# Performance work log

Measured on AMD Instinct MI355X. Metric: run time of the kernel, lower is better.

Reference implementation:

```python
import jax, jax.numpy as jnp
import numpy as np

N = 50000      # nodes
IN = 256       # in_feat
H = 4          # num_heads
DH = 64        # out_feat // num_heads
R = 6          # number of relations
E = 300000     # edges per relation
NEG_SLOPE = 0.2  # DGL GATConv leaky_relu slope


def setup_inputs() -> dict:
    key = jax.random.key(0)
    ks = jax.random.split(key, 7)
    x = jax.random.normal(ks[0], (N, IN), dtype=jnp.float32)
    W = jax.random.normal(ks[1], (R, IN, H * DH), dtype=jnp.float32) * (1.0 / np.sqrt(IN))
    attn_l = jax.random.normal(ks[2], (R, H, DH), dtype=jnp.float32) * 0.1
    attn_r = jax.random.normal(ks[3], (R, H, DH), dtype=jnp.float32) * 0.1
    bias = jax.random.normal(ks[4], (R, H * DH), dtype=jnp.float32) * 0.01
    src = jax.random.randint(ks[5], (R, E), 0, N, dtype=jnp.int32).astype(jnp.int64)
    dst = jax.random.randint(ks[6], (R, E), 0, N, dtype=jnp.int32).astype(jnp.int64)
    return {"x": x, "W": W, "attn_l": attn_l, "attn_r": attn_r, "bias": bias,
            "src": src, "dst": dst}


def reference(x, W, attn_l, attn_r, bias, src, dst):
    n = x.shape[0]
    r_total, h, dh = attn_l.shape
    out = jnp.zeros((n, h, dh), dtype=x.dtype)
    # small fixed loop over structurally-distinct relations (HeteroGraphConv)
    for r in range(r_total):
        feat = (x @ W[r]).reshape(n, h, dh)            # [N,H,Dh] shared src/dst proj
        el = jnp.sum(feat * attn_l[r], axis=-1)        # [N,H]
        er = jnp.sum(feat * attn_r[r], axis=-1)        # [N,H]
        s, d = src[r], dst[r]
        e = jax.nn.leaky_relu(el[s] + er[d], NEG_SLOPE)  # [E,H]
        # segmented softmax over incoming edges of each dst node
        m = jax.ops.segment_max(e, d, num_segments=n)    # [N,H]
        m = jnp.where(jnp.isfinite(m), m, 0.0)
        a = jnp.exp(e - m[d])                            # [E,H]
        z = jax.ops.segment_sum(a, d, num_segments=n)    # [N,H]
        alpha = a / jnp.maximum(z[d], 1e-9)              # [E,H]
        msg = alpha[:, :, None] * feat[s]                # [E,H,Dh]
        agg = jax.ops.segment_sum(msg, d, num_segments=n)  # [N,H,Dh]
        # GATConv: bias + activation(relu) per relation, HeteroGraphConv sums
        out = out + jax.nn.relu(agg + bias[r].reshape(h, dh))
    hcat = out.reshape(n, h * dh)                        # merge='cat' view
    return jax.nn.relu(hcat)                             # layer-level activation
```

## Files before the change

### kernel.cpp

```cpp
#include <hip/hip_runtime.h>

#define NN 50000
#define MP 50048
#define NH 4
#define NR 6
#define NE 300000
#define HD 256
#define SLOTS 32
#define CHUNKS 64
#define CHSZ ((NE + CHUNKS - 1) / CHUNKS)

typedef __attribute__((ext_vector_type(4))) float f32x4;
typedef __attribute__((ext_vector_type(8))) short bf16x8;

__device__ __forceinline__ short f2bf(float f) {
  unsigned u = __float_as_uint(f);
  unsigned r = (u + 0x7FFFu + ((u >> 16) & 1u)) >> 16;
  return (short)r;
}
__device__ __forceinline__ float bf2f_lo(unsigned d) {
  return __uint_as_float(d << 16);
}
__device__ __forceinline__ float bf2f_hi(unsigned d) {
  return __uint_as_float(d & 0xffff0000u);
}

#define GLOAD_LDS16(g, l)                                                     \
  __builtin_amdgcn_global_load_lds(                                           \
      (const __attribute__((address_space(1))) void*)(g),                     \
      (__attribute__((address_space(3))) void*)(l), 16, 0, 0)

__global__ __launch_bounds__(256) void cast_x_kernel(
    const float* __restrict__ x, short* __restrict__ xb, int n4) {
  const int i = blockIdx.x * 256 + threadIdx.x;
  if (i >= n4) return;
  const float4 v = ((const float4*)x)[i];
  short4 o;
  o.x = f2bf(v.x); o.y = f2bf(v.y); o.z = f2bf(v.z); o.w = f2bf(v.w);
  ((short4*)xb)[i] = o;
}

__global__ __launch_bounds__(256) void cast_wt_kernel(
    const float* __restrict__ W, short* __restrict__ wt) {
  const int o = blockIdx.x * 256 + threadIdx.x;
  if (o >= NR * 256 * 256) return;
  const int r = o >> 16;
  const int nrow = (o >> 8) & 255;
  const int k = o & 255;
  wt[o] = f2bf(W[r * 65536 + k * 256 + nrow]);
}

__global__ __launch_bounds__(256) void gemm_kernel(
    const short* __restrict__ xb,
    const short* __restrict__ wt_all,
    const float* __restrict__ attn_l,
    const float* __restrict__ attn_r,
    short* __restrict__ featb_all,
    float* __restrict__ el_all, float* __restrict__ er_all) {
  __shared__ short As[128 * 32];
  __shared__ short Bs[128 * 32];
  const int t = threadIdx.x;
  const int lane = t & 63;
  const int w = t >> 6;
  const int wm = w & 1, wn = w >> 1;
  const int row0 = blockIdx.x * 128;
  const int n0 = blockIdx.y * 128;
  const int r = blockIdx.z;
  const short* wt = wt_all + (size_t)r * 65536;
  short* featb = featb_all + (size_t)r * MP * 256;

  f32x4 acc[4][4];
#pragma unroll
  for (int mi = 0; mi < 4; ++mi)
#pragma unroll
    for (int ni = 0; ni < 4; ++ni) {
      f32x4 z = {0.f, 0.f, 0.f, 0.f};
      acc[mi][ni] = z;
    }

  const int c0 = t, c1 = 256 + t;
  int ar0 = row0 + (c0 >> 2); if (ar0 >= NN) ar0 = NN - 1;
  int ar1 = row0 + (c1 >> 2); if (ar1 >= NN) ar1 = NN - 1;
  const short* ag0 = xb + (size_t)ar0 * 256 + (c0 & 3) * 8;
  const short* ag1 = xb + (size_t)ar1 * 256 + (c1 & 3) * 8;
  const short* bg0 = wt + (size_t)(n0 + (c0 >> 2)) * 256 + (c0 & 3) * 8;
  const short* bg1 = wt + (size_t)(n0 + (c1 >> 2)) * 256 + (c1 & 3) * 8;
  short* la0 = As + c0 * 8;
  short* la1 = As + c1 * 8;
  short* lb0 = Bs + c0 * 8;
  short* lb1 = Bs + c1 * 8;

  const int ra = lane & 15;
  const int qa = (lane >> 4) * 8;

  for (int k0 = 0; k0 < 256; k0 += 32) {
    GLOAD_LDS16(ag0 + k0, la0);
    GLOAD_LDS16(ag1 + k0, la1);
    GLOAD_LDS16(bg0 + k0, lb0);
    GLOAD_LDS16(bg1 + k0, lb1);
    __syncthreads();
    bf16x8 af[4], bfr[4];
#pragma unroll
    for (int mi = 0; mi < 4; ++mi)
      af[mi] = *(const bf16x8*)&As[(wm * 64 + mi * 16 + ra) * 32 + qa];
#pragma unroll
    for (int ni = 0; ni < 4; ++ni)
      bfr[ni] = *(const bf16x8*)&Bs[(wn * 64 + ni * 16 + ra) * 32 + qa];
#pragma unroll
    for (int mi = 0; mi < 4; ++mi)
#pragma unroll
      for (int ni = 0; ni < 4; ++ni)
        acc[mi][ni] = __builtin_amdgcn_mfma_f32_16x16x32_bf16(
            af[mi], bfr[ni], acc[mi][ni], 0, 0, 0);
    __syncthreads();
  }

  const int h = (n0 >> 6) + wn;
  float alv[4], arv[4];
#pragma unroll
  for (int ni = 0; ni < 4; ++ni) {
    alv[ni] = attn_l[r * HD + h * 64 + ni * 16 + ra];
    arv[ni] = attn_r[r * HD + h * 64 + ni * 16 + ra];
  }
#pragma unroll
  for (int mi = 0; mi < 4; ++mi) {
#pragma unroll
    for (int j = 0; j < 4; ++j) {
      const int row = row0 + wm * 64 + mi * 16 + (lane >> 4) * 4 + j;
      float elp = 0.f, erp = 0.f;
#pragma unroll
      for (int ni = 0; ni < 4; ++ni) {
        const float v = acc[mi][ni][j];
        featb[(size_t)row * 256 + n0 + wn * 64 + ni * 16 + ra] = f2bf(v);
        elp = fmaf(v, alv[ni], elp);
        erp = fmaf(v, arv[ni], erp);
      }
#pragma unroll
      for (int m = 1; m < 16; m <<= 1) {
        elp += __shfl_xor(elp, m, 64);
        erp += __shfl_xor(erp, m, 64);
      }
      if (ra == 0 && row < NN) {
        el_all[((size_t)r * NN + row) * NH + h] = elp;
        er_all[((size_t)r * NN + row) * NH + h] = erp;
      }
    }
  }
}

__global__ __launch_bounds__(256) void pack_kernel(
    const int* __restrict__ src, const int* __restrict__ dst,
    unsigned* __restrict__ pe) {
  const int i = blockIdx.x * 256 + threadIdx.x;
  if (i < NR * NE)
    pe[i] = ((unsigned)dst[i] << 16) | (unsigned)src[i];
}

__global__ __launch_bounds__(256) void build_kernel(
    const unsigned* __restrict__ pe, int* __restrict__ deg,
    unsigned short* __restrict__ slots) {
  const int grp = blockIdx.x & 7;
  const int chunk = blockIdx.x >> 3;
  const int lo = chunk * CHSZ;
  const int hi = (lo + CHSZ < NE) ? lo + CHSZ : NE;
  const unsigned dlo = grp * (NN / 8);
  for (int r = 0; r < NR; ++r) {
    for (int i = lo + threadIdx.x; i < hi; i += 256) {
      const unsigned p = pe[(size_t)r * NE + i];
      const unsigned d = p >> 16;
      if (d - dlo < (unsigned)(NN / 8)) {
        const int g = r * NN + (int)d;
        const int sl = atomicAdd(&deg[g], 1);
        if (sl < SLOTS)
          slots[(size_t)g * SLOTS + sl] = (unsigned short)(p & 0xffffu);
      }
    }
  }
}

__global__ __launch_bounds__(256) void agg_kernel(
    const short* __restrict__ featb_all, const float* __restrict__ el_all,
    const float* __restrict__ er_all, const int* __restrict__ deg,
    const unsigned short* __restrict__ slots, const float* __restrict__ bias,
    float* __restrict__ out) {
  const int wid = (blockIdx.x * 256 + threadIdx.x) >> 6;
  const int lane = threadIdx.x & 63;
  if (wid >= NN) return;
  const int h = lane >> 4;
  const int c0 = lane * 4;

  float oacc[4] = {0.f, 0.f, 0.f, 0.f};
  const int wid_u = __builtin_amdgcn_readfirstlane(wid);

  for (int r = 0; r < NR; ++r) {
    const int g = r * NN + wid_u;
    int dg = __builtin_amdgcn_readfirstlane(deg[g]);
    dg = dg > SLOTS ? SLOTS : dg;
    const uint4* sp = (const uint4*)(slots + (size_t)g * SLOTS);
    const uint4 q0 = sp[0], q1 = sp[1], q2 = sp[2], q3 = sp[3];
    unsigned sdv[16];
    sdv[0]  = __builtin_amdgcn_readfirstlane(q0.x);
    sdv[1]  = __builtin_amdgcn_readfirstlane(q0.y);
    sdv[2]  = __builtin_amdgcn_readfirstlane(q0.z);
    sdv[3]  = __builtin_amdgcn_readfirstlane(q0.w);
    sdv[4]  = __builtin_amdgcn_readfirstlane(q1.x);
    sdv[5]  = __builtin_amdgcn_readfirstlane(q1.y);
    sdv[6]  = __builtin_amdgcn_readfirstlane(q1.z);
    sdv[7]  = __builtin_amdgcn_readfirstlane(q1.w);
    sdv[8]  = __builtin_amdgcn_readfirstlane(q2.x);
    sdv[9]  = __builtin_amdgcn_readfirstlane(q2.y);
    sdv[10] = __builtin_amdgcn_readfirstlane(q2.z);
    sdv[11] = __builtin_amdgcn_readfirstlane(q2.w);
    sdv[12] = __builtin_amdgcn_readfirstlane(q3.x);
    sdv[13] = __builtin_amdgcn_readfirstlane(q3.y);
    sdv[14] = __builtin_amdgcn_readfirstlane(q3.z);
    sdv[15] = __builtin_amdgcn_readfirstlane(q3.w);

    const float er_nh = er_all[(size_t)g * NH + h];
    const float* elr = el_all + (size_t)r * NN * NH;
    const short* fb = featb_all + (size_t)r * MP * 256;

    float z = 0.f;
    float acc[4] = {0.f, 0.f, 0.f, 0.f};

#pragma unroll
    for (int j0 = 0; j0 < SLOTS; j0 += 4) {
      if (j0 >= dg) break;
      float pv[4];
      uint2 rw[4];
#pragma unroll
      for (int k = 0; k < 4; ++k) {
        const int e = j0 + k;
        int s = (int)((e & 1) ? (sdv[e >> 1] >> 16) : (sdv[e >> 1] & 0xffffu));
        const bool v = e < dg;
        s = v ? s : 0;
        rw[k] = *(const uint2*)(fb + (size_t)s * 256 + c0);
        float ev = elr[s * NH + h] + er_nh;
        ev = fmaxf(ev, 0.2f * ev);
        pv[k] = v ? __expf(ev) : 0.f;
      }
#pragma unroll
      for (int k = 0; k < 4; ++k) {
        z += pv[k];
        acc[0] = fmaf(pv[k], bf2f_lo(rw[k].x), acc[0]);
        acc[1] = fmaf(pv[k], bf2f_hi(rw[k].x), acc[1]);
        acc[2] = fmaf(pv[k], bf2f_lo(rw[k].y), acc[2]);
        acc[3] = fmaf(pv[k], bf2f_hi(rw[k].y), acc[3]);
      }
    }

    const float inv = 1.f / fmaxf(z, 1e-9f);
    const float4 bv = *(const float4*)(bias + r * HD + c0);
    oacc[0] += fmaxf(fmaf(acc[0], inv, bv.x), 0.f);
    oacc[1] += fmaxf(fmaf(acc[1], inv, bv.y), 0.f);
    oacc[2] += fmaxf(fmaf(acc[2], inv, bv.z), 0.f);
    oacc[3] += fmaxf(fmaf(acc[3], inv, bv.w), 0.f);
  }

  float4 o4 = {oacc[0], oacc[1], oacc[2], oacc[3]};
  *(float4*)(out + (size_t)wid * 256 + c0) = o4;
}

extern "C" void kernel_launch(void* const* d_in, const int* in_sizes, int n_in,
                              void* d_out, int out_size, void* d_ws,
                              size_t ws_size, hipStream_t stream) {
  const float* x      = (const float*)d_in[0];
  const float* W      = (const float*)d_in[1];
  const float* attn_l = (const float*)d_in[2];
  const float* attn_r = (const float*)d_in[3];
  const float* bias   = (const float*)d_in[4];
  const int*   src    = (const int*)d_in[5];
  const int*   dst    = (const int*)d_in[6];
  float* out = (float*)d_out;

  char* p = (char*)d_ws;
  auto alloc = [&](size_t bytes) {
    char* r = p;
    p += (bytes + 255) & ~(size_t)255;
    return r;
  };
  short* xb    = (short*)alloc((size_t)NN * HD * 2);
  short* wt    = (short*)alloc((size_t)NR * 256 * 256 * 2);
  short* featb = (short*)alloc((size_t)NR * MP * 256 * 2);
  float* el    = (float*)alloc((size_t)NR * NN * NH * 4);
  float* er    = (float*)alloc((size_t)NR * NN * NH * 4);
  int*   deg   = (int*)alloc((size_t)NR * NN * 4);
  unsigned short* slots =
      (unsigned short*)alloc((size_t)NR * NN * SLOTS * 2);
  unsigned* pe = (unsigned*)alloc((size_t)NR * NE * 4);

  hipMemsetAsync(deg, 0, (size_t)NR * NN * 4, stream);

  cast_x_kernel<<<(NN * HD / 4 + 255) / 256, 256, 0, stream>>>(x, xb,
                                                               NN * HD / 4);
  cast_wt_kernel<<<(NR * 256 * 256 + 255) / 256, 256, 0, stream>>>(W, wt);
  pack_kernel<<<(NR * NE + 255) / 256, 256, 0, stream>>>(src, dst, pe);
  build_kernel<<<CHUNKS * 8, 256, 0, stream>>>(pe, deg, slots);
  gemm_kernel<<<dim3(MP / 128, 2, NR), 256, 0, stream>>>(xb, wt, attn_l,
                                                         attn_r, featb, el,
                                                         er);
  agg_kernel<<<(NN * 64) / 256, 256, 0, stream>>>(featb, el, er, deg, slots,
                                                  bias, out);
}
```

Measured before the change: 476.1 us.

## Merge edge pack into build, prefetch next relation slots, widen aggregation unroll

Drops the pack kernel and its packed-edge buffer. build_kernel now reads src/dst directly, one pass per chunk over 512 blocks, instead of 8 destination-range groups each rescanning every edge. The aggregation loop walks relations in reverse and prefetches the next relation's slots, degree and er while processing the current one. The inner edge unroll grows from 4 to 8 to put more gathers in flight. Risks are more atomic contention from the non-partitioned build and higher register pressure in agg_kernel.

```diff
diff --git a/kernel.cpp b/kernel.cpp
--- a/kernel.cpp
+++ b/kernel.cpp
@@ -7,8 +7,8 @@
 #define NE 300000
 #define HD 256
 #define SLOTS 32
-#define CHUNKS 64
-#define CHSZ ((NE + CHUNKS - 1) / CHUNKS)
+#define NB 512
+#define BSZ ((NE + NB - 1) / NB)
 
 typedef __attribute__((ext_vector_type(4))) float f32x4;
 typedef __attribute__((ext_vector_type(8))) short bf16x8;
@@ -148,32 +148,19 @@
   }
 }
 
-__global__ __launch_bounds__(256) void pack_kernel(
+__global__ __launch_bounds__(256) void build_kernel(
     const int* __restrict__ src, const int* __restrict__ dst,
-    unsigned* __restrict__ pe) {
-  const int i = blockIdx.x * 256 + threadIdx.x;
-  if (i < NR * NE)
-    pe[i] = ((unsigned)dst[i] << 16) | (unsigned)src[i];
-}
-
-__global__ __launch_bounds__(256) void build_kernel(
-    const unsigned* __restrict__ pe, int* __restrict__ deg,
-    unsigned short* __restrict__ slots) {
-  const int grp = blockIdx.x & 7;
-  const int chunk = blockIdx.x >> 3;
-  const int lo = chunk * CHSZ;
-  const int hi = (lo + CHSZ < NE) ? lo + CHSZ : NE;
-  const unsigned dlo = grp * (NN / 8);
+    int* __restrict__ deg, unsigned short* __restrict__ slots) {
+  const int lo = blockIdx.x * BSZ;
+  const int hi = (lo + BSZ < NE) ? lo + BSZ : NE;
   for (int r = 0; r < NR; ++r) {
     for (int i = lo + threadIdx.x; i < hi; i += 256) {
-      const unsigned p = pe[(size_t)r * NE + i];
-      const unsigned d = p >> 16;
-      if (d - dlo < (unsigned)(NN / 8)) {
-        const int g = r * NN + (int)d;
-        const int sl = atomicAdd(&deg[g], 1);
-        if (sl < SLOTS)
-          slots[(size_t)g * SLOTS + sl] = (unsigned short)(p & 0xffffu);
-      }
+      const int s = src[(size_t)r * NE + i];
+      const int d = dst[(size_t)r * NE + i];
+      const int g = r * NN + d;
+      const int sl = atomicAdd(&deg[g], 1);
+      if (sl < SLOTS)
+        slots[(size_t)g * SLOTS + sl] = (unsigned short)s;
     }
   }
 }
@@ -192,31 +179,46 @@
   float oacc[4] = {0.f, 0.f, 0.f, 0.f};
   const int wid_u = __builtin_amdgcn_readfirstlane(wid);
 
-  for (int r = 0; r < NR; ++r) {
-    const int g = r * NN + wid_u;
-    int dg = __builtin_amdgcn_readfirstlane(deg[g]);
-    dg = dg > SLOTS ? SLOTS : dg;
-    const uint4* sp = (const uint4*)(slots + (size_t)g * SLOTS);
-    const uint4 q0 = sp[0], q1 = sp[1], q2 = sp[2], q3 = sp[3];
+  {
+    const int g = (NR - 1) * NN + wid_u;
+    (void)g;
+  }
+  const int g_first = (NR - 1) * NN + wid_u;
+  const uint4* spf = (const uint4*)(slots + (size_t)g_first * SLOTS);
+  uint4 sq0 = spf[0], sq1 = spf[1], sq2 = spf[2], sq3 = spf[3];
+  int dgv = deg[g_first];
+  float erv = er_all[(size_t)g_first * NH + h];
+
+  for (int r = NR - 1; r >= 0; --r) {
+    const int dg0 = __builtin_amdgcn_readfirstlane(dgv);
+    const int dg = dg0 > SLOTS ? SLOTS : dg0;
     unsigned sdv[16];
-    sdv[0]  = __builtin_amdgcn_readfirstlane(q0.x);
-    sdv[1]  = __builtin_amdgcn_readfirstlane(q0.y);
-    sdv[2]  = __builtin_amdgcn_readfirstlane(q0.z);
-    sdv[3]  = __builtin_amdgcn_readfirstlane(q0.w);
-    sdv[4]  = __builtin_amdgcn_readfirstlane(q1.x);
-    sdv[5]  = __builtin_amdgcn_readfirstlane(q1.y);
-    sdv[6]  = __builtin_amdgcn_readfirstlane(q1.z);
-    sdv[7]  = __builtin_amdgcn_readfirstlane(q1.w);
-    sdv[8]  = __builtin_amdgcn_readfirstlane(q2.x);
-    sdv[9]  = __builtin_amdgcn_readfirstlane(q2.y);
-    sdv[10] = __builtin_amdgcn_readfirstlane(q2.z);
-    sdv[11] = __builtin_amdgcn_readfirstlane(q2.w);
-    sdv[12] = __builtin_amdgcn_readfirstlane(q3.x);
-    sdv[13] = __builtin_amdgcn_readfirstlane(q3.y);
-    sdv[14] = __builtin_amdgcn_readfirstlane(q3.z);
-    sdv[15] = __builtin_amdgcn_readfirstlane(q3.w);
-
-    const float er_nh = er_all[(size_t)g * NH + h];
+    sdv[0]  = __builtin_amdgcn_readfirstlane(sq0.x);
+    sdv[1]  = __builtin_amdgcn_readfirstlane(sq0.y);
+    sdv[2]  = __builtin_amdgcn_readfirstlane(sq0.z);
+    sdv[3]  = __builtin_amdgcn_readfirstlane(sq0.w);
+    sdv[4]  = __builtin_amdgcn_readfirstlane(sq1.x);
+    sdv[5]  = __builtin_amdgcn_readfirstlane(sq1.y);
+    sdv[6]  = __builtin_amdgcn_readfirstlane(sq1.z);
+    sdv[7]  = __builtin_amdgcn_readfirstlane(sq1.w);
+    sdv[8]  = __builtin_amdgcn_readfirstlane(sq2.x);
+    sdv[9]  = __builtin_amdgcn_readfirstlane(sq2.y);
+    sdv[10] = __builtin_amdgcn_readfirstlane(sq2.z);
+    sdv[11] = __builtin_amdgcn_readfirstlane(sq2.w);
+    sdv[12] = __builtin_amdgcn_readfirstlane(sq3.x);
+    sdv[13] = __builtin_amdgcn_readfirstlane(sq3.y);
+    sdv[14] = __builtin_amdgcn_readfirstlane(sq3.z);
+    sdv[15] = __builtin_amdgcn_readfirstlane(sq3.w);
+    const float er_nh = erv;
+
+    if (r > 0) {
+      const int g2 = (r - 1) * NN + wid_u;
+      const uint4* sp2 = (const uint4*)(slots + (size_t)g2 * SLOTS);
+      sq0 = sp2[0]; sq1 = sp2[1]; sq2 = sp2[2]; sq3 = sp2[3];
+      dgv = deg[g2];
+      erv = er_all[(size_t)g2 * NH + h];
+    }
+
     const float* elr = el_all + (size_t)r * NN * NH;
     const short* fb = featb_all + (size_t)r * MP * 256;
 
@@ -224,12 +226,12 @@
     float acc[4] = {0.f, 0.f, 0.f, 0.f};
 
 #pragma unroll
-    for (int j0 = 0; j0 < SLOTS; j0 += 4) {
+    for (int j0 = 0; j0 < SLOTS; j0 += 8) {
       if (j0 >= dg) break;
-      float pv[4];
-      uint2 rw[4];
-#pragma unroll
-      for (int k = 0; k < 4; ++k) {
+      float pv[8];
+      uint2 rw[8];
+#pragma unroll
+      for (int k = 0; k < 8; ++k) {
         const int e = j0 + k;
         int s = (int)((e & 1) ? (sdv[e >> 1] >> 16) : (sdv[e >> 1] & 0xffffu));
         const bool v = e < dg;
@@ -240,7 +242,7 @@
         pv[k] = v ? __expf(ev) : 0.f;
       }
 #pragma unroll
-      for (int k = 0; k < 4; ++k) {
+      for (int k = 0; k < 8; ++k) {
         z += pv[k];
         acc[0] = fmaf(pv[k], bf2f_lo(rw[k].x), acc[0]);
         acc[1] = fmaf(pv[k], bf2f_hi(rw[k].x), acc[1]);
@@ -287,15 +289,13 @@
   int*   deg   = (int*)alloc((size_t)NR * NN * 4);
   unsigned short* slots =
       (unsigned short*)alloc((size_t)NR * NN * SLOTS * 2);
-  unsigned* pe = (unsigned*)alloc((size_t)NR * NE * 4);
 
   hipMemsetAsync(deg, 0, (size_t)NR * NN * 4, stream);
 
   cast_x_kernel<<<(NN * HD / 4 + 255) / 256, 256, 0, stream>>>(x, xb,
                                                                NN * HD / 4);
   cast_wt_kernel<<<(NR * 256 * 256 + 255) / 256, 256, 0, stream>>>(W, wt);
-  pack_kernel<<<(NR * NE + 255) / 256, 256, 0, stream>>>(src, dst, pe);
-  build_kernel<<<CHUNKS * 8, 256, 0, stream>>>(pe, deg, slots);
+  build_kernel<<<NB, 256, 0, stream>>>(src, dst, deg, slots);
   gemm_kernel<<<dim3(MP / 128, 2, NR), 256, 0, stream>>>(xb, wt, attn_l,
                                                          attn_r, featb, el,
                                                          er);
```

Measured after the change: 473.3 us. Within noise of the previous version (-0.6%).
